# Kernel optimization log

Hardware: AMD Instinct MI355X
Metric: run time of the kernel (lower is better)

## Reference

```python
import jax, jax.numpy as jnp
import numpy as np

VOCAB = 50000
WORD_DIM = 300
HIDDEN = 300
REL = 3
B = 512        # batch of (premise, hypothesis) tree pairs
LEAVES = 256   # leaves per complete binary tree (depth 8)


def setup_inputs() -> dict:
    key = jax.random.key(0)
    ks = jax.random.split(key, 6)
    sc = lambda k, shape, s: jax.random.normal(k, shape, dtype=jnp.float32) * s
    return {
        "word_ids": jax.random.randint(ks[0], (B, 2, LEAVES), 0, VOCAB),
        "embedding": sc(ks[1], (VOCAB, WORD_DIM), 0.1),
        "W_leaf": sc(ks[2], (HIDDEN, WORD_DIM), 0.05),   # word2hidden (no bias)
        "W_h": sc(ks[3], (HIDDEN, 2 * HIDDEN), 0.05),    # hidden2hidden
        "b_h": jnp.zeros((HIDDEN,), jnp.float32),
        "W_cls": sc(ks[4], (REL, 2 * HIDDEN), 0.05),
        "b_cls": jnp.zeros((REL,), jnp.float32),
    }


def _encode_trees(word_ids, embedding, W_leaf, W_h, b_h):
    # word_ids: [B, 2, L] leaf token ids of complete binary trees.
    # Leaf: h = word2hidden(embedding(id))  (no bias, no activation)
    h = embedding[word_ids] @ W_leaf.T                     # [B, 2, L, H]
    # Postorder combine, level-synchronous: parent = hidden2hidden(cat(l, r))
    n = h.shape[2]
    while n > 1:
        left = h[:, :, 0::2, :]
        right = h[:, :, 1::2, :]
        h = jnp.concatenate([left, right], axis=-1) @ W_h.T + b_h
        n //= 2
    return h[:, :, 0, :]                                   # [B, 2, H] roots


def reference(word_ids, embedding, W_leaf, W_h, b_h, W_cls, b_cls):
    roots = _encode_trees(word_ids, embedding, W_leaf, W_h, b_h)  # [B, 2, H]
    feat = jax.nn.sigmoid(roots.reshape(roots.shape[0], -1))      # cat(p, h) -> [B, 2H]
    logits = feat @ W_cls.T + b_cls                               # [B, REL]
    return jax.nn.log_softmax(logits, axis=-1)
```

## Files before the change

### kernel.cpp

```cpp
#include <hip/hip_runtime.h>
#include <hip/hip_bf16.h>

typedef __hip_bfloat16 bf16;
typedef __attribute__((ext_vector_type(8))) short short8;
typedef __attribute__((ext_vector_type(4))) float float4v;
typedef __attribute__((ext_vector_type(4))) short short4v;

__device__ __forceinline__ short f2bs(float x) {
    bf16 b = __float2bfloat16(x);
    return *reinterpret_cast<short*>(&b);
}
__device__ __forceinline__ float bs2f(short s) {
    bf16 b = *reinterpret_cast<bf16*>(&s);
    return __bfloat162float(b);
}

#define GLL16(g, l) __builtin_amdgcn_global_load_lds(                      \
    (const __attribute__((address_space(1))) void*)(g),                    \
    (__attribute__((address_space(3))) void*)(l), 16, 0, 0)


__global__ __launch_bounds__(256) void conv_emb(
    const float* __restrict__ src, short* __restrict__ dst)
{
    const int idx = blockIdx.x * 256 + threadIdx.x;
    if (idx >= 50176 * 80) return;
    const int row = idx / 80;
    const int k4  = (idx - row * 80) * 4;
    short4v v = (short4v)0;
    if (row < 50000 && k4 < 300) {
        const float4v f = *reinterpret_cast<const float4v*>(
            src + (long)row * 300 + k4);
#pragma unroll
        for (int j = 0; j < 4; ++j) v[j] = f2bs(f[j]);
    }
    *(short4v*)&dst[(long)row * 320 + k4] = v;
}

__global__ __launch_bounds__(256) void conv_w(
    const float* __restrict__ W_h, const float* __restrict__ W_leaf,
    const float* __restrict__ b_h, short* __restrict__ Bh,
    short* __restrict__ Bleaf, float* __restrict__ biasp)
{
    const int idx = blockIdx.x * 256 + threadIdx.x;
    if (idx < 204800) {
        const int row = idx / 640, k = idx - row * 640;
        float v = 0.f;
        if (row < 300) {
            if (k < 300)                  v = W_h[row * 600 + k];
            else if (k >= 320 && k < 620) v = W_h[row * 600 + k - 20];
        }
        Bh[idx] = f2bs(v);
    } else if (idx < 307200) {
        const int i = idx - 204800;
        const int row = i / 320, k = i - row * 320;
        Bleaf[i] = (row < 300 && k < 300) ? f2bs(W_leaf[row * 300 + k])
                                          : (short)0;
    } else if (idx < 307520) {
        const int i = idx - 307200;
        biasp[i] = (i < 300) ? b_h[i] : 0.f;
    }
}

template <int KE, int GMODE, bool BIAS>
__global__ __launch_bounds__(256, 2) void mfma_gemm(
    const short* __restrict__ Xsrc, const int* __restrict__ wid,
    const short* __restrict__ emb, const short* __restrict__ Wp,
    const float* __restrict__ biasp, short* __restrict__ out)
{
    static_assert(GMODE != 2 || KE == 640, "pair-gather requires KE=640");
    __shared__ __align__(16) short As[2][128 * 32];
    __shared__ __align__(16) short Bs[2][320 * 32];

    const int tid  = threadIdx.x;
    const int lane = tid & 63;
    const int w    = tid >> 6;
    const int wm   = w >> 1, wn = w & 1;
    const long m0  = (long)blockIdx.x * 128;

    const int s_q   = lane & 3;
    const int r_off = lane >> 2;

    const char* gL[2];
    const char* gR[2];
#pragma unroll
    for (int j = 0; j < 2; ++j) {
        const int r = (w * 2 + j) * 16 + r_off;
        const int q = s_q ^ ((r >> 1) & 3);
        if (GMODE == 2) {
            const long node = m0 + r;
            gL[j] = (const char*)emb + (long)wid[2 * node]     * 640 + q * 16;
            gR[j] = (const char*)emb + (long)wid[2 * node + 1] * 640 + q * 16;
        } else {
            gL[j] = (const char*)Xsrc + (m0 + r) * (long)(KE * 2) + q * 16;
            gR[j] = gL[j];
        }
    }
    const char* gB[5];
#pragma unroll
    for (int j = 0; j < 5; ++j) {
        const int r = (w * 5 + j) * 16 + r_off;
        const int q = s_q ^ ((r >> 1) & 3);
        gB[j] = (const char*)Wp + r * (long)(KE * 2) + q * 16;
    }

    int oA[4];
#pragma unroll
    for (int t = 0; t < 4; ++t) {
        const int row = wm * 64 + t * 16 + (lane & 15);
        const int s   = (lane >> 4) ^ ((row >> 1) & 3);
        oA[t] = row * 32 + s * 8;
    }
    int oB[10];
#pragma unroll
    for (int u = 0; u < 10; ++u) {
        const int n = wn * 160 + u * 16 + (lane & 15);
        const int s = (lane >> 4) ^ ((n >> 1) & 3);
        oB[u] = n * 32 + s * 8;
    }

    auto stage = [&](int buf, int kc) {
        char* baseA = (char*)&As[buf][0];
        char* baseB = (char*)&Bs[buf][0];
        if (GMODE == 2) {
            const bool lft = (kc < 10);
            const int off = (lft ? kc : kc - 10) * 64;
            GLL16((lft ? gL[0] : gR[0]) + off, baseA + (w * 2 + 0) * 1024);
            GLL16((lft ? gL[1] : gR[1]) + off, baseA + (w * 2 + 1) * 1024);
        } else {
            const int off = kc * 64;
            GLL16(gL[0] + off, baseA + (w * 2 + 0) * 1024);
            GLL16(gL[1] + off, baseA + (w * 2 + 1) * 1024);
        }
        const int offb = kc * 64;
#pragma unroll
        for (int j = 0; j < 5; ++j)
            GLL16(gB[j] + offb, baseB + (w * 5 + j) * 1024);
    };

    float4v acc[4][10];
#pragma unroll
    for (int t = 0; t < 4; ++t)
#pragma unroll
        for (int u = 0; u < 10; ++u) acc[t][u] = (float4v)0.f;

    const int NCH = KE / 32;
    stage(0, 0);
    for (int kc = 0; kc < NCH; ++kc) {
        const int cur = kc & 1;
        if (kc + 1 < NCH) {
            stage(cur ^ 1, kc + 1);
            asm volatile("s_waitcnt vmcnt(7)" ::: "memory");
        } else {
            asm volatile("s_waitcnt vmcnt(0)" ::: "memory");
        }
        __builtin_amdgcn_s_barrier();
        __builtin_amdgcn_sched_barrier(0);

        const short* bA = &As[cur][0];
        const short* bB = &Bs[cur][0];
        short8 a[4], b[10];
#pragma unroll
        for (int t = 0; t < 4; ++t) a[t] = *(const short8*)(bA + oA[t]);
#pragma unroll
        for (int u = 0; u < 10; ++u) b[u] = *(const short8*)(bB + oB[u]);
#pragma unroll
        for (int u = 0; u < 10; ++u)
#pragma unroll
            for (int t = 0; t < 4; ++t)
                acc[t][u] = __builtin_amdgcn_mfma_f32_16x16x32_bf16(
                    a[t], b[u], acc[t][u], 0, 0, 0);
        __builtin_amdgcn_s_barrier();
    }

#pragma unroll
    for (int u = 0; u < 10; ++u) {
        const int c = wn * 160 + u * 16 + (lane & 15);
        const float bv = BIAS ? biasp[c] : 0.f;
#pragma unroll
        for (int t = 0; t < 4; ++t) {
            const long mb = m0 + wm * 64 + t * 16 + (lane >> 4) * 4;
#pragma unroll
            for (int r4 = 0; r4 < 4; ++r4)
                out[(mb + r4) * 320 + c] = f2bs(acc[t][u][r4] + bv);
        }
    }
}

__global__ __launch_bounds__(512, 1) void mfma_bk(
    const short* __restrict__ Xsrc, const short* __restrict__ Wp,
    const float* __restrict__ biasp, short* __restrict__ out)
{
    __shared__ __align__(16) short As[4 * 128 * 32];
    __shared__ __align__(16) short Bs[4 * 320 * 32];

    const int tid  = threadIdx.x;
    const int lane = tid & 63;
    const int w    = tid >> 6;
    const int wm   = w >> 2;
    const int wn   = w & 3;
    const long m0  = (long)blockIdx.x * 128;

    const int s_q   = lane & 3;
    const int r_off = lane >> 2;

    const int rA = w * 16 + r_off;
    const int qA = s_q ^ ((rA >> 1) & 3);
    const char* gA = (const char*)Xsrc + (m0 + rA) * (long)(640 * 2) + qA * 16;

    const char* gB[10];
    int pB[10], loB[10];
#pragma unroll
    for (int i = 0; i < 10; ++i) {
        const int gid = w * 10 + i;
        const int p   = gid / 20;
        const int grp = gid - p * 20;
        const int r   = grp * 16 + r_off;
        const int q   = s_q ^ ((r >> 1) & 3);
        gB[i]  = (const char*)Wp + r * (long)(640 * 2) + q * 16;
        pB[i]  = p;
        loB[i] = p * 20480 + grp * 1024;
    }

    int oA[4];
#pragma unroll
    for (int t = 0; t < 4; ++t) {
        const int row = wm * 64 + t * 16 + (lane & 15);
        const int s   = (lane >> 4) ^ ((row >> 1) & 3);
        oA[t] = row * 32 + s * 8;
    }
    int oB[5];
#pragma unroll
    for (int u = 0; u < 5; ++u) {
        const int n = wn * 80 + u * 16 + (lane & 15);
        const int s = (lane >> 4) ^ ((n >> 1) & 3);
        oB[u] = n * 32 + s * 8;
    }

    float4v acc[4][5];
#pragma unroll
    for (int t = 0; t < 4; ++t)
#pragma unroll
        for (int u = 0; u < 5; ++u) acc[t][u] = (float4v)0.f;

    for (int kc = 0; kc < 5; ++kc) {
#pragma unroll
        for (int p = 0; p < 4; ++p) {
            const int pk = kc * 4 + p;
            GLL16(gA + (long)pk * 64, (char*)As + p * 8192 + w * 1024);
        }
#pragma unroll
        for (int i = 0; i < 10; ++i)
            GLL16(gB[i] + (long)(kc * 4 + pB[i]) * 64, (char*)Bs + loB[i]);

        asm volatile("s_waitcnt vmcnt(0)" ::: "memory");
        __builtin_amdgcn_s_barrier();
        __builtin_amdgcn_sched_barrier(0);

#pragma unroll
        for (int p = 0; p < 4; ++p) {
            const short* bA = As + p * 4096;
            const short* bB = Bs + p * 10240;
            short8 a[4], b[5];
#pragma unroll
            for (int t = 0; t < 4; ++t) a[t] = *(const short8*)(bA + oA[t]);
#pragma unroll
            for (int u = 0; u < 5; ++u) b[u] = *(const short8*)(bB + oB[u]);
#pragma unroll
            for (int u = 0; u < 5; ++u)
#pragma unroll
                for (int t = 0; t < 4; ++t)
                    acc[t][u] = __builtin_amdgcn_mfma_f32_16x16x32_bf16(
                        a[t], b[u], acc[t][u], 0, 0, 0);
        }
        __builtin_amdgcn_s_barrier();
    }

#pragma unroll
    for (int u = 0; u < 5; ++u) {
        const int c = wn * 80 + u * 16 + (lane & 15);
        const float bv = biasp[c];
#pragma unroll
        for (int t = 0; t < 4; ++t) {
            const long mb = m0 + wm * 64 + t * 16 + (lane >> 4) * 4;
#pragma unroll
            for (int r4 = 0; r4 < 4; ++r4)
                out[(mb + r4) * 320 + c] = f2bs(acc[t][u][r4] + bv);
        }
    }
}

__global__ __launch_bounds__(64) void cls_kernel(
    const short* __restrict__ roots, const float* __restrict__ W_cls,
    const float* __restrict__ b_cls, float* __restrict__ out)
{
    const int b    = blockIdx.x;
    const int lane = threadIdx.x;
    const short* row = roots + (long)b * 640;

    float a0 = 0.f, a1 = 0.f, a2 = 0.f;
#pragma unroll
    for (int i = 0; i < 10; ++i) {
        const int k = lane + 64 * i;
        if (k < 600) {
            const int col = (k < 300) ? k : k + 20;
            const float f = 1.f / (1.f + __expf(-bs2f(row[col])));
            a0 += f * W_cls[k];
            a1 += f * W_cls[600 + k];
            a2 += f * W_cls[1200 + k];
        }
    }
#pragma unroll
    for (int off = 32; off > 0; off >>= 1) {
        a0 += __shfl_down(a0, off);
        a1 += __shfl_down(a1, off);
        a2 += __shfl_down(a2, off);
    }
    if (lane == 0) {
        const float l0 = a0 + b_cls[0];
        const float l1 = a1 + b_cls[1];
        const float l2 = a2 + b_cls[2];
        const float m  = fmaxf(l0, fmaxf(l1, l2));
        const float s  = __expf(l0 - m) + __expf(l1 - m) + __expf(l2 - m);
        const float ls = m + __logf(s);
        out[b * 3 + 0] = l0 - ls;
        out[b * 3 + 1] = l1 - ls;
        out[b * 3 + 2] = l2 - ls;
    }
}

extern "C" void kernel_launch(void* const* d_in, const int* in_sizes, int n_in,
                              void* d_out, int out_size, void* d_ws, size_t ws_size,
                              hipStream_t stream)
{
    const int*   wid    = (const int*)d_in[0];
    const float* emb    = (const float*)d_in[1];
    const float* W_leaf = (const float*)d_in[2];
    const float* W_h    = (const float*)d_in[3];
    const float* b_h    = (const float*)d_in[4];
    const float* W_cls  = (const float*)d_in[5];
    const float* b_cls  = (const float*)d_in[6];
    float* outp = (float*)d_out;

    (void)in_sizes; (void)n_in; (void)out_size; (void)ws_size;

    char* ws = (char*)d_ws;
    short* bufA   = (short*)(ws);
    short* bufB   = (short*)(ws + 83886080);
    short* emb_bf = (short*)(ws + 83886080);
    short* Hv     = (short*)(ws + 125829120);
    short* Bleaf  = (short*)(ws + 157941760);
    short* Bh     = (short*)(ws + 158146560);
    float* biasp  = (float*)(ws + 158556160);

    conv_emb<<<(50176 * 80) / 256, 256, 0, stream>>>(emb, emb_bf);
    conv_w  <<<(307520 + 255) / 256, 256, 0, stream>>>(
        W_h, W_leaf, b_h, Bh, Bleaf, biasp);

    mfma_gemm<320, 0, false><<<50176 / 128, 256, 0, stream>>>(
        emb_bf, nullptr, nullptr, Bleaf, biasp, Hv);

    mfma_gemm<640, 2, true><<<131072 / 128, 256, 0, stream>>>(
        nullptr, wid, Hv, Bh, biasp, bufA);

    short* cur = bufA;
    short* nxt = bufB;
    int nodes = 65536;
    for (int l = 0; l < 7; ++l) {
        mfma_bk<<<nodes / 128, 512, 0, stream>>>(cur, Bh, biasp, nxt);
        short* t = cur; cur = nxt; nxt = t;
        nodes >>= 1;
    }

    cls_kernel<<<512, 64, 0, stream>>>(cur, W_cls, b_cls, outp);
}
```

Measured before the change: 354.6 us.

## Fuse tree-level GEMMs and classifier into one cooperative persistent kernel

Replaces the seven per-level mfma_bk launches and the separate classifier launch with a single cooperative kernel of 256 blocks. The blocks loop over tiles at each tree level and use grid.sync between levels. The classifier then runs in the first two waves of each block. This removes launch overhead and the tail gaps between small late-level kernels, at the cost of grid-wide barriers and the early levels running on only 256 persistent blocks.

New measurement: 563.7 us. 1.59x slower.

```diff
diff --git a/kernel.cpp b/kernel.cpp
--- a/kernel.cpp
+++ b/kernel.cpp
@@ -1,5 +1,8 @@
 #include <hip/hip_runtime.h>
 #include <hip/hip_bf16.h>
+#include <hip/hip_cooperative_groups.h>
+
+namespace cg = cooperative_groups;
 
 typedef __hip_bfloat16 bf16;
 typedef __attribute__((ext_vector_type(8))) short short8;
@@ -187,26 +190,23 @@
     }
 }
 
-__global__ __launch_bounds__(512, 1) void mfma_bk(
-    const short* __restrict__ Xsrc, const short* __restrict__ Wp,
-    const float* __restrict__ biasp, short* __restrict__ out)
+__global__ __launch_bounds__(512, 1) void tree_tail(
+    short* bufA, short* bufB, const short* __restrict__ Wp,
+    const float* __restrict__ biasp, const float* __restrict__ W_cls,
+    const float* __restrict__ b_cls, float* __restrict__ outp)
 {
     __shared__ __align__(16) short As[4 * 128 * 32];
     __shared__ __align__(16) short Bs[4 * 320 * 32];
+
+    cg::grid_group grid = cg::this_grid();
 
     const int tid  = threadIdx.x;
     const int lane = tid & 63;
     const int w    = tid >> 6;
     const int wm   = w >> 2;
     const int wn   = w & 3;
-    const long m0  = (long)blockIdx.x * 128;
-
     const int s_q   = lane & 3;
     const int r_off = lane >> 2;
-
-    const int rA = w * 16 + r_off;
-    const int qA = s_q ^ ((rA >> 1) & 3);
-    const char* gA = (const char*)Xsrc + (m0 + rA) * (long)(640 * 2) + qA * 16;
 
     const char* gB[10];
     int pB[10], loB[10];
@@ -217,11 +217,13 @@
         const int grp = gid - p * 20;
         const int r   = grp * 16 + r_off;
         const int q   = s_q ^ ((r >> 1) & 3);
-        gB[i]  = (const char*)Wp + r * (long)(640 * 2) + q * 16;
+        gB[i]  = (const char*)Wp + r * 1280L + q * 16;
         pB[i]  = p;
         loB[i] = p * 20480 + grp * 1024;
     }
 
+    const int rA = w * 16 + r_off;
+    const int qA = s_q ^ ((rA >> 1) & 3);
     int oA[4];
 #pragma unroll
     for (int t = 0; t < 4; ++t) {
@@ -237,95 +239,106 @@
         oB[u] = n * 32 + s * 8;
     }
 
-    float4v acc[4][5];
-#pragma unroll
-    for (int t = 0; t < 4; ++t)
-#pragma unroll
-        for (int u = 0; u < 5; ++u) acc[t][u] = (float4v)0.f;
-
-    for (int kc = 0; kc < 5; ++kc) {
-#pragma unroll
-        for (int p = 0; p < 4; ++p) {
-            const int pk = kc * 4 + p;
-            GLL16(gA + (long)pk * 64, (char*)As + p * 8192 + w * 1024);
-        }
-#pragma unroll
-        for (int i = 0; i < 10; ++i)
-            GLL16(gB[i] + (long)(kc * 4 + pB[i]) * 64, (char*)Bs + loB[i]);
-
-        asm volatile("s_waitcnt vmcnt(0)" ::: "memory");
-        __builtin_amdgcn_s_barrier();
-        __builtin_amdgcn_sched_barrier(0);
-
-#pragma unroll
-        for (int p = 0; p < 4; ++p) {
-            const short* bA = As + p * 4096;
-            const short* bB = Bs + p * 10240;
-            short8 a[4], b[5];
-#pragma unroll
-            for (int t = 0; t < 4; ++t) a[t] = *(const short8*)(bA + oA[t]);
-#pragma unroll
-            for (int u = 0; u < 5; ++u) b[u] = *(const short8*)(bB + oB[u]);
-#pragma unroll
-            for (int u = 0; u < 5; ++u)
-#pragma unroll
-                for (int t = 0; t < 4; ++t)
-                    acc[t][u] = __builtin_amdgcn_mfma_f32_16x16x32_bf16(
-                        a[t], b[u], acc[t][u], 0, 0, 0);
-        }
-        __builtin_amdgcn_s_barrier();
-    }
-
-#pragma unroll
-    for (int u = 0; u < 5; ++u) {
-        const int c = wn * 80 + u * 16 + (lane & 15);
-        const float bv = biasp[c];
-#pragma unroll
-        for (int t = 0; t < 4; ++t) {
-            const long mb = m0 + wm * 64 + t * 16 + (lane >> 4) * 4;
-#pragma unroll
-            for (int r4 = 0; r4 < 4; ++r4)
-                out[(mb + r4) * 320 + c] = f2bs(acc[t][u][r4] + bv);
-        }
-    }
-}
-
-__global__ __launch_bounds__(64) void cls_kernel(
-    const short* __restrict__ roots, const float* __restrict__ W_cls,
-    const float* __restrict__ b_cls, float* __restrict__ out)
-{
-    const int b    = blockIdx.x;
-    const int lane = threadIdx.x;
-    const short* row = roots + (long)b * 640;
-
-    float a0 = 0.f, a1 = 0.f, a2 = 0.f;
-#pragma unroll
-    for (int i = 0; i < 10; ++i) {
-        const int k = lane + 64 * i;
-        if (k < 600) {
-            const int col = (k < 300) ? k : k + 20;
-            const float f = 1.f / (1.f + __expf(-bs2f(row[col])));
-            a0 += f * W_cls[k];
-            a1 += f * W_cls[600 + k];
-            a2 += f * W_cls[1200 + k];
-        }
-    }
-#pragma unroll
-    for (int off = 32; off > 0; off >>= 1) {
-        a0 += __shfl_down(a0, off);
-        a1 += __shfl_down(a1, off);
-        a2 += __shfl_down(a2, off);
-    }
-    if (lane == 0) {
-        const float l0 = a0 + b_cls[0];
-        const float l1 = a1 + b_cls[1];
-        const float l2 = a2 + b_cls[2];
-        const float m  = fmaxf(l0, fmaxf(l1, l2));
-        const float s  = __expf(l0 - m) + __expf(l1 - m) + __expf(l2 - m);
-        const float ls = m + __logf(s);
-        out[b * 3 + 0] = l0 - ls;
-        out[b * 3 + 1] = l1 - ls;
-        out[b * 3 + 2] = l2 - ls;
+    short* cur = bufA;
+    short* nxt = bufB;
+    int nodes = 65536;
+    for (int l = 0; l < 7; ++l) {
+        const int nt = nodes >> 7;
+        for (int t0 = blockIdx.x; t0 < nt; t0 += 256) {
+            const long m0 = (long)t0 * 128;
+            const char* gA = (const char*)cur + (m0 + rA) * 1280L + qA * 16;
+
+            float4v acc[4][5];
+#pragma unroll
+            for (int t = 0; t < 4; ++t)
+#pragma unroll
+                for (int u = 0; u < 5; ++u) acc[t][u] = (float4v)0.f;
+
+            for (int kc = 0; kc < 5; ++kc) {
+#pragma unroll
+                for (int p = 0; p < 4; ++p)
+                    GLL16(gA + (long)(kc * 4 + p) * 64,
+                          (char*)As + p * 8192 + w * 1024);
+#pragma unroll
+                for (int i = 0; i < 10; ++i)
+                    GLL16(gB[i] + (long)(kc * 4 + pB[i]) * 64,
+                          (char*)Bs + loB[i]);
+
+                asm volatile("s_waitcnt vmcnt(0)" ::: "memory");
+                __builtin_amdgcn_s_barrier();
+                __builtin_amdgcn_sched_barrier(0);
+
+#pragma unroll
+                for (int p = 0; p < 4; ++p) {
+                    const short* bA = As + p * 4096;
+                    const short* bB = Bs + p * 10240;
+                    short8 a[4], b[5];
+#pragma unroll
+                    for (int t = 0; t < 4; ++t)
+                        a[t] = *(const short8*)(bA + oA[t]);
+#pragma unroll
+                    for (int u = 0; u < 5; ++u)
+                        b[u] = *(const short8*)(bB + oB[u]);
+#pragma unroll
+                    for (int u = 0; u < 5; ++u)
+#pragma unroll
+                        for (int t = 0; t < 4; ++t)
+                            acc[t][u] =
+                                __builtin_amdgcn_mfma_f32_16x16x32_bf16(
+                                    a[t], b[u], acc[t][u], 0, 0, 0);
+                }
+                __builtin_amdgcn_s_barrier();
+            }
+
+#pragma unroll
+            for (int u = 0; u < 5; ++u) {
+                const int c = wn * 80 + u * 16 + (lane & 15);
+                const float bv = biasp[c];
+#pragma unroll
+                for (int t = 0; t < 4; ++t) {
+                    const long mb = m0 + wm * 64 + t * 16 + (lane >> 4) * 4;
+#pragma unroll
+                    for (int r4 = 0; r4 < 4; ++r4)
+                        nxt[(mb + r4) * 320 + c] = f2bs(acc[t][u][r4] + bv);
+                }
+            }
+        }
+        grid.sync();
+        short* tswap = cur; cur = nxt; nxt = tswap;
+        nodes >>= 1;
+    }
+    if (w < 2) {
+        const int b = blockIdx.x * 2 + w;
+        const short* row = cur + (long)b * 640;
+        float a0 = 0.f, a1 = 0.f, a2 = 0.f;
+#pragma unroll
+        for (int i = 0; i < 10; ++i) {
+            const int k = lane + 64 * i;
+            if (k < 600) {
+                const int col = (k < 300) ? k : k + 20;
+                const float f = 1.f / (1.f + __expf(-bs2f(row[col])));
+                a0 += f * W_cls[k];
+                a1 += f * W_cls[600 + k];
+                a2 += f * W_cls[1200 + k];
+            }
+        }
+#pragma unroll
+        for (int off = 32; off > 0; off >>= 1) {
+            a0 += __shfl_down(a0, off);
+            a1 += __shfl_down(a1, off);
+            a2 += __shfl_down(a2, off);
+        }
+        if (lane == 0) {
+            const float l0 = a0 + b_cls[0];
+            const float l1 = a1 + b_cls[1];
+            const float l2 = a2 + b_cls[2];
+            const float m  = fmaxf(l0, fmaxf(l1, l2));
+            const float s  = __expf(l0 - m) + __expf(l1 - m) + __expf(l2 - m);
+            const float ls = m + __logf(s);
+            outp[b * 3 + 0] = l0 - ls;
+            outp[b * 3 + 1] = l1 - ls;
+            outp[b * 3 + 2] = l2 - ls;
+        }
     }
 }
 
@@ -363,14 +376,13 @@
     mfma_gemm<640, 2, true><<<131072 / 128, 256, 0, stream>>>(
         nullptr, wid, Hv, Bh, biasp, bufA);
 
-    short* cur = bufA;
-    short* nxt = bufB;
-    int nodes = 65536;
-    for (int l = 0; l < 7; ++l) {
-        mfma_bk<<<nodes / 128, 512, 0, stream>>>(cur, Bh, biasp, nxt);
-        short* t = cur; cur = nxt; nxt = t;
-        nodes >>= 1;
-    }
-
-    cls_kernel<<<512, 64, 0, stream>>>(cur, W_cls, b_cls, outp);
-}
+    {
+        short* tA = bufA; short* tB = bufB;
+        const short* tW = Bh; const float* tb = biasp;
+        const float* tc = W_cls; const float* td = b_cls;
+        float* to = outp;
+        void* ka[] = {&tA, &tB, &tW, &tb, &tc, &td, &to};
+        hipLaunchCooperativeKernel((void*)tree_tail, dim3(256), dim3(512),
+                                   ka, 0, stream);
+    }
+}
```

## Fuse upper tree levels and classifier into one per-pair subtree kernel

Applied to the files above, without the earlier changes.

Replaces the seven per-level GEMM launches and the separate classifier kernel with two kernels. One generic GEMM computes the first internal level, then a single subtree kernel per batch element runs the remaining six levels. It keeps intermediates in LDS ping-pong buffers with a swizzled layout and finishes with sigmoid, classifier and log-softmax. This removes the launch overhead and the global round-trips for the small upper levels. In exchange each block reloads the full weight matrix per level, and the tiny upper levels leave the MFMA tiles mostly idle.

New measurement: 343.8 us. 3.1% less time.

```diff
diff --git a/kernel.cpp b/kernel.cpp
--- a/kernel.cpp
+++ b/kernel.cpp
@@ -187,145 +187,153 @@
     }
 }
 
-__global__ __launch_bounds__(512, 1) void mfma_bk(
-    const short* __restrict__ Xsrc, const short* __restrict__ Wp,
-    const float* __restrict__ biasp, short* __restrict__ out)
-{
-    __shared__ __align__(16) short As[4 * 128 * 32];
-    __shared__ __align__(16) short Bs[4 * 320 * 32];
+template<int MA, bool STREAM, bool TOROOTS>
+__device__ __forceinline__ void tree_level(
+    const int w, const int lane,
+    const short* Ain, short* Aout, short* Bs, short* Astage,
+    const char* gA, const char* gB0, const char* gB1, const char* gB2,
+    const char* gB3, const char* gB4, const float* __restrict__ biasp)
+{
+    constexpr int MT  = (MA + 15) / 16;
+    constexpr int TPW = MT * 5;
+    const int lrow = lane & 15;
+    const int hi   = lane >> 4;
+
+    float4v acc[TPW];
+#pragma unroll
+    for (int t = 0; t < TPW; ++t) acc[t] = (float4v)0.f;
+
+    for (int kc = 0; kc < 20; ++kc) {
+        GLL16(gB0 + kc * 64, (char*)Bs + (w * 5 + 0) * 1024);
+        GLL16(gB1 + kc * 64, (char*)Bs + (w * 5 + 1) * 1024);
+        GLL16(gB2 + kc * 64, (char*)Bs + (w * 5 + 2) * 1024);
+        GLL16(gB3 + kc * 64, (char*)Bs + (w * 5 + 3) * 1024);
+        GLL16(gB4 + kc * 64, (char*)Bs + (w * 5 + 4) * 1024);
+        if (STREAM)
+            GLL16(gA + (kc >= 10 ? 640 : 0) + (kc % 10) * 64,
+                  (char*)Astage + w * 1024);
+        asm volatile("s_waitcnt vmcnt(0)" ::: "memory");
+        __builtin_amdgcn_s_barrier();
+        __builtin_amdgcn_sched_barrier(0);
+
+#pragma unroll
+        for (int t = 0; t < TPW; ++t) {
+            const int g  = w + t * 4;
+            const int mt = g / 20, nt = g % 20;
+            int row = mt * 16 + lrow;
+            if (MA < 16) row = (lrow < MA) ? lrow : 0;
+            const int sa = hi ^ ((row >> 1) & 3);
+            const short* pa = STREAM
+                ? (Astage + row * 32 + sa * 8)
+                : (Ain + kc * (MA * 32) + row * 32 + sa * 8);
+            const int n  = nt * 16 + lrow;
+            const int sb = hi ^ ((n >> 1) & 3);
+            const short8 a = *(const short8*)pa;
+            const short8 b = *(const short8*)(Bs + n * 32 + sb * 8);
+            acc[t] = __builtin_amdgcn_mfma_f32_16x16x32_bf16(
+                a, b, acc[t], 0, 0, 0);
+        }
+        __builtin_amdgcn_s_barrier();
+    }
+
+#pragma unroll
+    for (int t = 0; t < TPW; ++t) {
+        const int g  = w + t * 4;
+        const int mt = g / 20, nt = g % 20;
+        const int c  = nt * 16 + lrow;
+        const float bv = biasp[c];
+#pragma unroll
+        for (int r4 = 0; r4 < 4; ++r4) {
+            const int mb = mt * 16 + hi * 4 + r4;
+            if (mb < MA) {
+                const short v = f2bs(acc[t][r4] + bv);
+                if (TOROOTS) {
+                    Aout[mb * 320 + c] = v;
+                } else {
+                    constexpr int MN = MA / 2;
+                    const int p  = (mb & 1) * 10 + (c >> 5);
+                    const int m2 = mb >> 1;
+                    const int q  = (c >> 3) & 3;
+                    Aout[p * (MN * 32) + m2 * 32 +
+                         (q ^ ((m2 >> 1) & 3)) * 8 + (c & 7)] = v;
+                }
+            }
+        }
+    }
+    __syncthreads();
+}
+
+__global__ __launch_bounds__(256, 2) void subtree(
+    const short* __restrict__ L2in, const short* __restrict__ Wp,
+    const float* __restrict__ biasp, const float* __restrict__ W_cls,
+    const float* __restrict__ b_cls, float* __restrict__ outp)
+{
+    __shared__ __align__(16) short Bs[320 * 32];
+    __shared__ __align__(16) short AX[20 * 32 * 32];
+    __shared__ __align__(16) short AY[10240];
 
     const int tid  = threadIdx.x;
     const int lane = tid & 63;
     const int w    = tid >> 6;
-    const int wm   = w >> 2;
-    const int wn   = w & 3;
-    const long m0  = (long)blockIdx.x * 128;
-
     const int s_q   = lane & 3;
     const int r_off = lane >> 2;
-
-    const int rA = w * 16 + r_off;
-    const int qA = s_q ^ ((rA >> 1) & 3);
-    const char* gA = (const char*)Xsrc + (m0 + rA) * (long)(640 * 2) + qA * 16;
-
-    const char* gB[10];
-    int pB[10], loB[10];
-#pragma unroll
-    for (int i = 0; i < 10; ++i) {
-        const int gid = w * 10 + i;
-        const int p   = gid / 20;
-        const int grp = gid - p * 20;
-        const int r   = grp * 16 + r_off;
-        const int q   = s_q ^ ((r >> 1) & 3);
-        gB[i]  = (const char*)Wp + r * (long)(640 * 2) + q * 16;
-        pB[i]  = p;
-        loB[i] = p * 20480 + grp * 1024;
-    }
-
-    int oA[4];
-#pragma unroll
-    for (int t = 0; t < 4; ++t) {
-        const int row = wm * 64 + t * 16 + (lane & 15);
-        const int s   = (lane >> 4) ^ ((row >> 1) & 3);
-        oA[t] = row * 32 + s * 8;
-    }
-    int oB[5];
-#pragma unroll
-    for (int u = 0; u < 5; ++u) {
-        const int n = wn * 80 + u * 16 + (lane & 15);
-        const int s = (lane >> 4) ^ ((n >> 1) & 3);
-        oB[u] = n * 32 + s * 8;
-    }
-
-    float4v acc[4][5];
-#pragma unroll
-    for (int t = 0; t < 4; ++t)
-#pragma unroll
-        for (int u = 0; u < 5; ++u) acc[t][u] = (float4v)0.f;
-
-    for (int kc = 0; kc < 5; ++kc) {
-#pragma unroll
-        for (int p = 0; p < 4; ++p) {
-            const int pk = kc * 4 + p;
-            GLL16(gA + (long)pk * 64, (char*)As + p * 8192 + w * 1024);
-        }
-#pragma unroll
-        for (int i = 0; i < 10; ++i)
-            GLL16(gB[i] + (long)(kc * 4 + pB[i]) * 64, (char*)Bs + loB[i]);
-
-        asm volatile("s_waitcnt vmcnt(0)" ::: "memory");
-        __builtin_amdgcn_s_barrier();
-        __builtin_amdgcn_sched_barrier(0);
-
-#pragma unroll
-        for (int p = 0; p < 4; ++p) {
-            const short* bA = As + p * 4096;
-            const short* bB = Bs + p * 10240;
-            short8 a[4], b[5];
-#pragma unroll
-            for (int t = 0; t < 4; ++t) a[t] = *(const short8*)(bA + oA[t]);
-#pragma unroll
-            for (int u = 0; u < 5; ++u) b[u] = *(const short8*)(bB + oB[u]);
-#pragma unroll
-            for (int u = 0; u < 5; ++u)
-#pragma unroll
-                for (int t = 0; t < 4; ++t)
-                    acc[t][u] = __builtin_amdgcn_mfma_f32_16x16x32_bf16(
-                        a[t], b[u], acc[t][u], 0, 0, 0);
-        }
-        __builtin_amdgcn_s_barrier();
-    }
-
-#pragma unroll
-    for (int u = 0; u < 5; ++u) {
-        const int c = wn * 80 + u * 16 + (lane & 15);
-        const float bv = biasp[c];
-#pragma unroll
-        for (int t = 0; t < 4; ++t) {
-            const long mb = m0 + wm * 64 + t * 16 + (lane >> 4) * 4;
-#pragma unroll
-            for (int r4 = 0; r4 < 4; ++r4)
-                out[(mb + r4) * 320 + c] = f2bs(acc[t][u][r4] + bv);
-        }
-    }
-}
-
-__global__ __launch_bounds__(64) void cls_kernel(
-    const short* __restrict__ roots, const float* __restrict__ W_cls,
-    const float* __restrict__ b_cls, float* __restrict__ out)
-{
-    const int b    = blockIdx.x;
-    const int lane = threadIdx.x;
-    const short* row = roots + (long)b * 640;
-
-    float a0 = 0.f, a1 = 0.f, a2 = 0.f;
-#pragma unroll
-    for (int i = 0; i < 10; ++i) {
-        const int k = lane + 64 * i;
-        if (k < 600) {
-            const int col = (k < 300) ? k : k + 20;
-            const float f = 1.f / (1.f + __expf(-bs2f(row[col])));
-            a0 += f * W_cls[k];
-            a1 += f * W_cls[600 + k];
-            a2 += f * W_cls[1200 + k];
-        }
-    }
-#pragma unroll
-    for (int off = 32; off > 0; off >>= 1) {
-        a0 += __shfl_down(a0, off);
-        a1 += __shfl_down(a1, off);
-        a2 += __shfl_down(a2, off);
-    }
-    if (lane == 0) {
-        const float l0 = a0 + b_cls[0];
-        const float l1 = a1 + b_cls[1];
-        const float l2 = a2 + b_cls[2];
-        const float m  = fmaxf(l0, fmaxf(l1, l2));
-        const float s  = __expf(l0 - m) + __expf(l1 - m) + __expf(l2 - m);
-        const float ls = m + __logf(s);
-        out[b * 3 + 0] = l0 - ls;
-        out[b * 3 + 1] = l1 - ls;
-        out[b * 3 + 2] = l2 - ls;
+    const long base = (long)blockIdx.x * 128;
+
+    const char* gB[5];
+#pragma unroll
+    for (int j = 0; j < 5; ++j) {
+        const int r = (w * 5 + j) * 16 + r_off;
+        const int q = s_q ^ ((r >> 1) & 3);
+        gB[j] = (const char*)Wp + r * 1280L + q * 16;
+    }
+    const int rS = w * 16 + r_off;
+    const int qS = s_q ^ ((rS >> 1) & 3);
+    const char* gA3 = (const char*)L2in + (base + 2 * rS) * 640 + qS * 16;
+
+    tree_level<64, true,  false>(w, lane, nullptr, AX, Bs, AY, gA3,
+                                 gB[0], gB[1], gB[2], gB[3], gB[4], biasp);
+    tree_level<32, false, false>(w, lane, AX, AY, Bs, nullptr, nullptr,
+                                 gB[0], gB[1], gB[2], gB[3], gB[4], biasp);
+    tree_level<16, false, false>(w, lane, AY, AX, Bs, nullptr, nullptr,
+                                 gB[0], gB[1], gB[2], gB[3], gB[4], biasp);
+    tree_level<8,  false, false>(w, lane, AX, AY, Bs, nullptr, nullptr,
+                                 gB[0], gB[1], gB[2], gB[3], gB[4], biasp);
+    tree_level<4,  false, false>(w, lane, AY, AX, Bs, nullptr, nullptr,
+                                 gB[0], gB[1], gB[2], gB[3], gB[4], biasp);
+    tree_level<2,  false, true >(w, lane, AX, AY, Bs, nullptr, nullptr,
+                                 gB[0], gB[1], gB[2], gB[3], gB[4], biasp);
+
+    if (w == 0) {
+        float a0 = 0.f, a1 = 0.f, a2 = 0.f;
+#pragma unroll
+        for (int i = 0; i < 10; ++i) {
+            const int k = lane + 64 * i;
+            if (k < 600) {
+                const int col = (k < 300) ? k : (320 + k - 300);
+                const float f = 1.f / (1.f + __expf(-bs2f(AY[col])));
+                a0 += f * W_cls[k];
+                a1 += f * W_cls[600 + k];
+                a2 += f * W_cls[1200 + k];
+            }
+        }
+#pragma unroll
+        for (int off = 32; off > 0; off >>= 1) {
+            a0 += __shfl_down(a0, off);
+            a1 += __shfl_down(a1, off);
+            a2 += __shfl_down(a2, off);
+        }
+        if (lane == 0) {
+            const int b = blockIdx.x;
+            const float l0 = a0 + b_cls[0];
+            const float l1 = a1 + b_cls[1];
+            const float l2 = a2 + b_cls[2];
+            const float m  = fmaxf(l0, fmaxf(l1, l2));
+            const float s  = __expf(l0 - m) + __expf(l1 - m) + __expf(l2 - m);
+            const float ls = m + __logf(s);
+            outp[b * 3 + 0] = l0 - ls;
+            outp[b * 3 + 1] = l1 - ls;
+            outp[b * 3 + 2] = l2 - ls;
+        }
     }
 }
 
@@ -363,14 +371,8 @@
     mfma_gemm<640, 2, true><<<131072 / 128, 256, 0, stream>>>(
         nullptr, wid, Hv, Bh, biasp, bufA);
 
-    short* cur = bufA;
-    short* nxt = bufB;
-    int nodes = 65536;
-    for (int l = 0; l < 7; ++l) {
-        mfma_bk<<<nodes / 128, 512, 0, stream>>>(cur, Bh, biasp, nxt);
-        short* t = cur; cur = nxt; nxt = t;
-        nodes >>= 1;
-    }
-
-    cls_kernel<<<512, 64, 0, stream>>>(cur, W_cls, b_cls, outp);
-}
+    mfma_gemm<640, 0, true><<<65536 / 128, 256, 0, stream>>>(
+        bufA, nullptr, nullptr, Bh, biasp, bufB);
+
+    subtree<<<512, 256, 0, stream>>>(bufB, Bh, biasp, W_cls, b_cls, outp);
+}
```
